# Optimization experiments

Measured on AMD Instinct MI355X. Metric: run time of the kernel, lower is better.

## Reference

```python
import itertools
import jax, jax.numpy as jnp
import numpy as np

EPS = 1.1920928955078125e-07  # torch.finfo(float32).eps, used by torchmetrics SI-SNR


def setup_inputs() -> dict:
    key = jax.random.key(0)
    k1, k2 = jax.random.split(key)
    B, S, T = 32, 2, 256000
    preds = jax.random.normal(k1, (B, S, T), dtype=jnp.float32)
    targets = jax.random.normal(k2, (B, S, T), dtype=jnp.float32)
    return {"preds": preds, "targets": targets}


def _pit_sisnr_loss(preds, targets):
    # preds, targets: [B, S, T]
    B, S, T = preds.shape
    # torchmetrics SI-SNR zero-means both signals along time
    p = preds - jnp.mean(preds, axis=-1, keepdims=True)
    t = targets - jnp.mean(targets, axis=-1, keepdims=True)
    # pairwise statistics: pred i vs target j
    dot = jnp.einsum('bit,bjt->bij', p, t)          # <p_i, t_j>        [B,S,S]
    tt = jnp.sum(t * t, axis=-1)                    # ||t_j||^2          [B,S]
    pp = jnp.sum(p * p, axis=-1)                    # ||p_i||^2          [B,S]
    alpha = dot / (tt[:, None, :] + EPS)            # projection scale   [B,S,S]
    s_target = alpha * alpha * tt[:, None, :]       # ||alpha * t||^2
    # ||p - alpha*t||^2 expanded (no [B,S,S,T] intermediate)
    noise = pp[:, :, None] - 2.0 * alpha * dot + s_target
    sisnr = 10.0 * jnp.log10((s_target + EPS) / (noise + EPS))  # [B,S,S]
    # PIT: max over all speaker permutations of the mean matched SI-SNR
    perms = np.array(list(itertools.permutations(range(S))))    # [P,S]
    rows = np.arange(S)[None, :]                                # [1,S]
    perm_scores = sisnr[:, rows, perms].mean(axis=-1)           # [B,P]
    best = perm_scores.max(axis=-1)                             # [B]
    return -jnp.mean(best)


def reference(preds, targets):
    return _pit_sisnr_loss(preds, targets)
```

## Files before the change

kernel.cpp:

```cpp
#include <hip/hip_runtime.h>

#define EPS 1.1920928955078125e-07f

#define BB 32
#define TT 256000
#define CHUNKS 50
#define T4 (TT / 4)
#define CHUNK (T4 / CHUNKS)
#define SEGS_PER_WAVE 5
#define NBLK (BB * CHUNKS)


__global__ __launch_bounds__(256, 4) void pit_partials(
    const float* __restrict__ preds, const float* __restrict__ targets,
    float* __restrict__ ws)
{
    const int b = blockIdx.x / CHUNKS;
    const int c = blockIdx.x % CHUNKS;
    const int lane = threadIdx.x & 63;
    const int wave = threadIdx.x >> 6;

    const float4* p0 = (const float4*)(preds   + (size_t)(b * 2 + 0) * TT);
    const float4* p1 = (const float4*)(preds   + (size_t)(b * 2 + 1) * TT);
    const float4* t0 = (const float4*)(targets + (size_t)(b * 2 + 0) * TT);
    const float4* t1 = (const float4*)(targets + (size_t)(b * 2 + 1) * TT);

    float acc[12];
#pragma unroll
    for (int k = 0; k < 12; ++k) acc[k] = 0.f;

    const int base = c * CHUNK + wave * (SEGS_PER_WAVE * 64) + lane;

    float4 a0 = p0[base], a1 = p1[base], b0 = t0[base], b1 = t1[base];
#pragma unroll
    for (int s = 0; s < SEGS_PER_WAVE; ++s) {
        float4 na0, na1, nb0, nb1;
        if (s + 1 < SEGS_PER_WAVE) {
            const int i = base + (s + 1) * 64;
            na0 = p0[i]; na1 = p1[i]; nb0 = t0[i]; nb1 = t1[i];
        }
#pragma unroll
        for (int e = 0; e < 4; ++e) {
            float u0 = (&a0.x)[e], u1 = (&a1.x)[e];
            float v0 = (&b0.x)[e], v1 = (&b1.x)[e];
            acc[0]  += u0;       acc[1]  += u1;
            acc[2]  += v0;       acc[3]  += v1;
            acc[4]  += u0 * u0;  acc[5]  += u1 * u1;
            acc[6]  += v0 * v0;  acc[7]  += v1 * v1;
            acc[8]  += u0 * v0;  acc[9]  += u0 * v1;
            acc[10] += u1 * v0;  acc[11] += u1 * v1;
        }
        a0 = na0; a1 = na1; b0 = nb0; b1 = nb1;
    }

#pragma unroll
    for (int k = 0; k < 12; ++k) {
        float v = acc[k];
        for (int off = 32; off > 0; off >>= 1) v += __shfl_down(v, off);
        acc[k] = v;
    }

    __shared__ float lds[4][12];
    if (lane == 0) {
#pragma unroll
        for (int k = 0; k < 12; ++k) lds[wave][k] = acc[k];
    }
    __syncthreads();

    if (threadIdx.x < 12) {
        float v = lds[0][threadIdx.x] + lds[1][threadIdx.x]
                + lds[2][threadIdx.x] + lds[3][threadIdx.x];
        ws[(size_t)blockIdx.x * 12 + threadIdx.x] = v;
    }
}

__global__ __launch_bounds__(256) void pit_final(
    const float* __restrict__ ws, float* __restrict__ out)
{
    __shared__ float sums[BB * 12];
    __shared__ float bests[BB];

    for (int s = threadIdx.x; s < BB * 12; s += 256) {
        const int b = s / 12;
        const int k = s % 12;
        float v = 0.f;
        const float* base = ws + (size_t)(b * CHUNKS) * 12 + k;
#pragma unroll 10
        for (int c = 0; c < CHUNKS; ++c) v += base[(size_t)c * 12];
        sums[s] = v;
    }
    __syncthreads();

    if (threadIdx.x < BB) {
        const float* w = sums + threadIdx.x * 12;
        const float invT = 1.0f / (float)TT;
        float pp0 = w[4] - w[0] * w[0] * invT;
        float pp1 = w[5] - w[1] * w[1] * invT;
        float tt0 = w[6] - w[2] * w[2] * invT;
        float tt1 = w[7] - w[3] * w[3] * invT;
        float d00 = w[8]  - w[0] * w[2] * invT;
        float d01 = w[9]  - w[0] * w[3] * invT;
        float d10 = w[10] - w[1] * w[2] * invT;
        float d11 = w[11] - w[1] * w[3] * invT;

        auto sisnr = [](float dot, float pp, float tt) -> float {
            float alpha = dot / (tt + EPS);
            float st    = alpha * alpha * tt;
            float noise = pp - 2.0f * alpha * dot + st;
            return 10.0f * log10f((st + EPS) / (noise + EPS));
        };
        float s00 = sisnr(d00, pp0, tt0);
        float s01 = sisnr(d01, pp0, tt1);
        float s10 = sisnr(d10, pp1, tt0);
        float s11 = sisnr(d11, pp1, tt1);

        float perm0 = 0.5f * (s00 + s11);
        float perm1 = 0.5f * (s01 + s10);
        bests[threadIdx.x] = fmaxf(perm0, perm1);
    }
    __syncthreads();

    if (threadIdx.x == 0) {
        float acc = 0.f;
#pragma unroll
        for (int b = 0; b < BB; ++b) acc += bests[b];
        out[0] = -acc / (float)BB;
    }
}

extern "C" void kernel_launch(void* const* d_in, const int* in_sizes, int n_in,
                              void* d_out, int out_size, void* d_ws, size_t ws_size,
                              hipStream_t stream)
{
    const float* preds   = (const float*)d_in[0];
    const float* targets = (const float*)d_in[1];
    float* out = (float*)d_out;
    float* ws  = (float*)d_ws;

    pit_partials<<<dim3(NBLK), dim3(256), 0, stream>>>(preds, targets, ws);
    pit_final<<<dim3(1), dim3(256), 0, stream>>>(ws, out);
}
```

Before: 147.3 us.

## Stage per-stream chunks into LDS via global_load_lds before reducing

Each wave now streams one of the four input rows (two preds, two targets) straight into shared memory with direct global-to-LDS loads, and the block then reads the staged float4 tiles to build the twelve partial sums. The grid grows to 125 chunks of 512 float4 per batch and the occupancy hint is dropped. The aim is more loads in flight and fewer vector registers tied up holding loaded data. The cost is 32 KB of LDS per block, which limits resident blocks per CU, plus an extra barrier and more partials for the final kernel to sum.

Result: slower. 156.7 us (+6.4%).

```diff
diff --git a/kernel.cpp b/kernel.cpp
--- a/kernel.cpp
+++ b/kernel.cpp
@@ -4,41 +4,49 @@
 
 #define BB 32
 #define TT 256000
-#define CHUNKS 50
 #define T4 (TT / 4)
-#define CHUNK (T4 / CHUNKS)
-#define SEGS_PER_WAVE 5
+#define CHUNKS 125
+#define CHUNK 512
 #define NBLK (BB * CHUNKS)
+#define STAGE_INSTR (CHUNK / 64)
 
 
-__global__ __launch_bounds__(256, 4) void pit_partials(
+__global__ __launch_bounds__(256) void pit_partials(
     const float* __restrict__ preds, const float* __restrict__ targets,
     float* __restrict__ ws)
 {
-    const int b = blockIdx.x / CHUNKS;
-    const int c = blockIdx.x % CHUNKS;
+    __shared__ float4 tile[4][CHUNK];
+
+    const int b    = blockIdx.x / CHUNKS;
+    const int c    = blockIdx.x % CHUNKS;
     const int lane = threadIdx.x & 63;
     const int wave = threadIdx.x >> 6;
 
-    const float4* p0 = (const float4*)(preds   + (size_t)(b * 2 + 0) * TT);
-    const float4* p1 = (const float4*)(preds   + (size_t)(b * 2 + 1) * TT);
-    const float4* t0 = (const float4*)(targets + (size_t)(b * 2 + 0) * TT);
-    const float4* t1 = (const float4*)(targets + (size_t)(b * 2 + 1) * TT);
+    const float* gbase = (wave < 2)
+        ? preds   + (size_t)(b * 2 + (wave & 1)) * TT
+        : targets + (size_t)(b * 2 + (wave & 1)) * TT;
+    const float4* src = (const float4*)gbase + (size_t)c * CHUNK;
+
+#pragma unroll
+    for (int j = 0; j < STAGE_INSTR; ++j) {
+        __builtin_amdgcn_global_load_lds(
+            (const __attribute__((address_space(1))) void*)(src + j * 64 + lane),
+            (__attribute__((address_space(3))) void*)&tile[wave][j * 64],
+            16, 0, 0);
+    }
+    __syncthreads();
 
     float acc[12];
 #pragma unroll
     for (int k = 0; k < 12; ++k) acc[k] = 0.f;
 
-    const int base = c * CHUNK + wave * (SEGS_PER_WAVE * 64) + lane;
-
-    float4 a0 = p0[base], a1 = p1[base], b0 = t0[base], b1 = t1[base];
 #pragma unroll
-    for (int s = 0; s < SEGS_PER_WAVE; ++s) {
-        float4 na0, na1, nb0, nb1;
-        if (s + 1 < SEGS_PER_WAVE) {
-            const int i = base + (s + 1) * 64;
-            na0 = p0[i]; na1 = p1[i]; nb0 = t0[i]; nb1 = t1[i];
-        }
+    for (int it = 0; it < CHUNK / 256; ++it) {
+        const int i = (int)threadIdx.x + it * 256;
+        float4 a0 = tile[0][i];
+        float4 a1 = tile[1][i];
+        float4 b0 = tile[2][i];
+        float4 b1 = tile[3][i];
 #pragma unroll
         for (int e = 0; e < 4; ++e) {
             float u0 = (&a0.x)[e], u1 = (&a1.x)[e];
@@ -50,7 +58,6 @@
             acc[8]  += u0 * v0;  acc[9]  += u0 * v1;
             acc[10] += u1 * v0;  acc[11] += u1 * v1;
         }
-        a0 = na0; a1 = na1; b0 = nb0; b1 = nb1;
     }
 
 #pragma unroll
@@ -60,16 +67,17 @@
         acc[k] = v;
     }
 
-    __shared__ float lds[4][12];
+    __syncthreads();
+    float* red = (float*)tile;
     if (lane == 0) {
 #pragma unroll
-        for (int k = 0; k < 12; ++k) lds[wave][k] = acc[k];
+        for (int k = 0; k < 12; ++k) red[wave * 12 + k] = acc[k];
     }
     __syncthreads();
 
     if (threadIdx.x < 12) {
-        float v = lds[0][threadIdx.x] + lds[1][threadIdx.x]
-                + lds[2][threadIdx.x] + lds[3][threadIdx.x];
+        float v = red[0 * 12 + threadIdx.x] + red[1 * 12 + threadIdx.x]
+                + red[2 * 12 + threadIdx.x] + red[3 * 12 + threadIdx.x];
         ws[(size_t)blockIdx.x * 12 + threadIdx.x] = v;
     }
 }
@@ -85,7 +93,6 @@
         const int k = s % 12;
         float v = 0.f;
         const float* base = ws + (size_t)(b * CHUNKS) * 12 + k;
-#pragma unroll 10
         for (int c = 0; c < CHUNKS; ++c) v += base[(size_t)c * 12];
         sums[s] = v;
     }
```
